# Kernel tuning notes

Hardware: AMD Instinct MI355X
Metric: run time of the kernel (lower is better)

## Reference

```python
import math
import jax, jax.numpy as jnp
import numpy as np

# --- dimensions ---
B = 32          # crystals
N_PER = 96      # building blocks per crystal
M = B * N_PER   # total nodes = 3072
H = 8           # no_heads
CH = 16         # c_hidden
PQK = 8         # no_qk_points
PV = 12         # no_v_points
CS = 256        # c_s
CZ = 128        # c_z
E = B * N_PER * N_PER  # dense intra-crystal edges = 294912
INV_SOFTPLUS_1 = 0.541324854612918


def _quat_to_rot(q):
    """Unit quaternion [M,4] -> rotation matrices [M,3,3]."""
    w, x, y, z = q[:, 0], q[:, 1], q[:, 2], q[:, 3]
    R = jnp.stack([
        1 - 2 * (y * y + z * z), 2 * (x * y - w * z), 2 * (x * z + w * y),
        2 * (x * y + w * z), 1 - 2 * (x * x + z * z), 2 * (y * z - w * x),
        2 * (x * z - w * y), 2 * (y * z + w * x), 1 - 2 * (x * x + y * y)],
        axis=-1)
    return R.reshape(-1, 3, 3)


def _lin_params(k, din, dout):
    kw, kb = jax.random.split(k)
    W = jax.random.normal(kw, (din, dout), jnp.float32) / np.sqrt(din).astype(np.float32)
    b = jax.random.normal(kb, (dout,), jnp.float32) * 0.01
    return W, b


def setup_inputs() -> dict:
    key = jax.random.key(0)
    ks = jax.random.split(key, 16)
    s = jax.random.normal(ks[0], (M, CS), jnp.float32)
    z = jax.random.normal(ks[1], (E, CZ), jnp.float32)
    quat = jax.random.normal(ks[2], (M, 4), jnp.float32)
    rot = _quat_to_rot(quat / jnp.linalg.norm(quat, axis=-1, keepdims=True))
    trans = jax.random.normal(ks[3], (M, 3), jnp.float32)
    L = jax.random.normal(ks[4], (B, 6), jnp.float32)
    # block-diagonal fully-connected intra-crystal edges
    i = np.repeat(np.arange(N_PER), N_PER)
    j = np.tile(np.arange(N_PER), N_PER)
    off = (np.arange(B) * N_PER)[:, None]
    src = (off + i[None, :]).reshape(-1)
    tgt = (off + j[None, :]).reshape(-1)
    edge_index = jnp.asarray(np.stack([src, tgt]), jnp.int32)
    num_bbs = jnp.full((B,), N_PER, jnp.int32)
    Wq, bq = _lin_params(ks[5], CS, H * CH)
    Wkv, bkv = _lin_params(ks[6], CS, 2 * H * CH)
    Wqp, bqp = _lin_params(ks[7], CS, H * PQK * 3)
    Wkvp, bkvp = _lin_params(ks[8], CS, H * (PQK + PV) * 3)
    Wb, bb = _lin_params(ks[9], CZ, H)
    Wl, bl = _lin_params(ks[10], 6, H)
    head_weights = INV_SOFTPLUS_1 + 0.1 * jax.random.normal(ks[11], (H,), jnp.float32)
    Wout, bout = _lin_params(ks[12], H * (CH + 3 * PV) + 6, CS)
    return dict(s=s, z=z, rot=rot, trans=trans, L=L,
                Wq=Wq, bq=bq, Wkv=Wkv, bkv=bkv, Wqp=Wqp, bqp=bqp,
                Wkvp=Wkvp, bkvp=bkvp, Wb=Wb, bb=bb, Wl=Wl, bl=bl,
                head_weights=head_weights, Wout=Wout, bout=bout,
                edge_index=edge_index, num_bbs=num_bbs)


def reference(s, z, rot, trans, L, Wq, bq, Wkv, bkv, Wqp, bqp, Wkvp, bkvp,
              Wb, bb, Wl, bl, head_weights, Wout, bout, edge_index, num_bbs):
    src, tgt = edge_index[0], edge_index[1]
    # scalar q/k/v
    q = (s @ Wq + bq).reshape(M, H, CH)
    kv = (s @ Wkv + bkv).reshape(M, H, 2 * CH)
    k, v = kv[..., :CH], kv[..., CH:]

    # point q/k/v: torch splits last dim into 3 coord chunks then stacks -> reshape (M,3,H,P)
    def points(W, bias, P):
        p = (s @ W + bias).reshape(M, 3, H, P).transpose(0, 2, 3, 1)  # [M,H,P,3]
        return jnp.einsum('mij,mhpj->mhpi', rot, p) + trans[:, None, None, :]

    q_pts = points(Wqp, bqp, PQK)                 # [M,H,PQK,3] in global frame
    kv_pts = points(Wkvp, bkvp, PQK + PV)         # [M,H,PQK+PV,3]
    k_pts, v_pts = kv_pts[:, :, :PQK], kv_pts[:, :, PQK:]

    b_pair = z @ Wb + bb                          # [E,H]
    batch_idx = jnp.repeat(jnp.arange(B), num_bbs, total_repeat_length=M)  # node -> crystal
    l_nodes = (L @ Wl + bl)[batch_idx]            # [M,H]

    # fused multi-term attention logits
    a = jnp.einsum('ehc,ehc->eh', q[tgt], k[src]) * math.sqrt(1.0 / (4 * CH))
    a = a + 0.5 * b_pair + 0.5 * l_nodes[src]
    disp = q_pts[tgt] - k_pts[src]                # [E,H,PQK,3]
    pt_att = jnp.sum(disp * disp, axis=-1)        # [E,H,PQK]
    hw = jax.nn.softplus(head_weights) * math.sqrt(1.0 / (4 * (PQK * 9.0 / 2)))
    a = a - 0.5 * jnp.sum(pt_att * hw[None, :, None], axis=-1)

    # segment softmax over incoming edges of each target node
    amax = jax.ops.segment_max(a, tgt, num_segments=M)
    ex = jnp.exp(a - amax[tgt])
    denom = jax.ops.segment_sum(ex, tgt, num_segments=M)
    attn = ex / denom[tgt]                        # [E,H]

    o = jax.ops.segment_sum(attn[..., None] * v[src], tgt, num_segments=M)
    o = o.reshape(M, H * CH)
    o_pt = jax.ops.segment_sum(attn[..., None, None] * v_pts[src], tgt, num_segments=M)
    o_pt = o_pt.reshape(M, H * PV, 3)
    o_l = L[batch_idx]                            # [M,6]
    o_feats = jnp.concatenate([o, o_pt[..., 0], o_pt[..., 1], o_pt[..., 2], o_l], axis=-1)
    return o_feats @ Wout + bout                  # [M,CS]
```

## Files before the change

### kernel.cpp

```cpp
#include <hip/hip_runtime.h>
#include <math.h>

#define B_    32
#define NPER_ 96
#define M_    3072
#define H_    8
#define CH_   16
#define PQK_  8
#define PV_   12
#define CS_   256
#define CZ_   128
#define E_    294912
#define NCAT_ 1056

template <bool ALIGN_A>
__global__ __launch_bounds__(256) void gemm64(const float* __restrict__ A,
                                              const float* __restrict__ W,
                                              const float* __restrict__ bias,
                                              float* __restrict__ C,
                                              int N, int K) {
  __shared__ float As[16][68];
  __shared__ float Bs[16][64];
  const int tid = threadIdx.x;
  const int tx = tid & 15, ty = tid >> 4;
  const int row0 = blockIdx.y * 64, col0 = blockIdx.x * 64;
  float acc[4][4] = {};

  for (int k0 = 0; k0 < K; k0 += 16) {
    {
      const int m = tid >> 2, k4 = (tid & 3) * 4;
      const int gk = k0 + k4;
      float a0 = 0.f, a1 = 0.f, a2 = 0.f, a3 = 0.f;
      if (ALIGN_A) {
        const float4 av = *reinterpret_cast<const float4*>(A + (size_t)(row0 + m) * K + gk);
        a0 = av.x; a1 = av.y; a2 = av.z; a3 = av.w;
      } else {
        const float* ap = A + (size_t)(row0 + m) * K;
        if (gk + 0 < K) a0 = ap[gk + 0];
        if (gk + 1 < K) a1 = ap[gk + 1];
        if (gk + 2 < K) a2 = ap[gk + 2];
        if (gk + 3 < K) a3 = ap[gk + 3];
      }
      As[k4 + 0][m] = a0; As[k4 + 1][m] = a1; As[k4 + 2][m] = a2; As[k4 + 3][m] = a3;
    }
    {
      const int kk = tid >> 4, n4 = (tid & 15) * 4;
      const int gk = k0 + kk, gn = col0 + n4;
      float4 bv; bv.x = 0.f; bv.y = 0.f; bv.z = 0.f; bv.w = 0.f;
      if (gk < K) {
        if (gn + 3 < N) {
          bv = *reinterpret_cast<const float4*>(W + (size_t)gk * N + gn);
        } else {
          const float* wp = W + (size_t)gk * N;
          if (gn + 0 < N) bv.x = wp[gn + 0];
          if (gn + 1 < N) bv.y = wp[gn + 1];
          if (gn + 2 < N) bv.z = wp[gn + 2];
          if (gn + 3 < N) bv.w = wp[gn + 3];
        }
      }
      *reinterpret_cast<float4*>(&Bs[kk][n4]) = bv;
    }
    __syncthreads();
#pragma unroll
    for (int kk = 0; kk < 16; ++kk) {
      const float4 a_ = *reinterpret_cast<const float4*>(&As[kk][ty * 4]);
      const float4 b_ = *reinterpret_cast<const float4*>(&Bs[kk][tx * 4]);
      acc[0][0] += a_.x * b_.x; acc[0][1] += a_.x * b_.y; acc[0][2] += a_.x * b_.z; acc[0][3] += a_.x * b_.w;
      acc[1][0] += a_.y * b_.x; acc[1][1] += a_.y * b_.y; acc[1][2] += a_.y * b_.z; acc[1][3] += a_.y * b_.w;
      acc[2][0] += a_.z * b_.x; acc[2][1] += a_.z * b_.y; acc[2][2] += a_.z * b_.z; acc[2][3] += a_.z * b_.w;
      acc[3][0] += a_.w * b_.x; acc[3][1] += a_.w * b_.y; acc[3][2] += a_.w * b_.z; acc[3][3] += a_.w * b_.w;
    }
    __syncthreads();
  }
#pragma unroll
  for (int i2 = 0; i2 < 4; ++i2) {
    const int gr = row0 + ty * 4 + i2;
#pragma unroll
    for (int j2 = 0; j2 < 4; ++j2) {
      const int gn = col0 + tx * 4 + j2;
      if (gn < N) C[(size_t)gr * N + gn] = acc[i2][j2] + bias[gn];
    }
  }
}

__global__ __launch_bounds__(256) void pack_w(const float* __restrict__ Wq,
                                              const float* __restrict__ Wkv,
                                              const float* __restrict__ Wqp,
                                              const float* __restrict__ Wkvp,
                                              const float* __restrict__ bq,
                                              const float* __restrict__ bkv,
                                              const float* __restrict__ bqp,
                                              const float* __restrict__ bkvp,
                                              float* __restrict__ Wcat,
                                              float* __restrict__ bcat) {
  const int t = blockIdx.x * 256 + threadIdx.x;
  if (t < 256 * NCAT_) {
    const int k = t / NCAT_, n = t - k * NCAT_;
    float v;
    if (n < 128)      v = Wq [k * 128 + n];
    else if (n < 384) v = Wkv[k * 256 + n - 128];
    else if (n < 576) v = Wqp[k * 192 + n - 384];
    else              v = Wkvp[k * 480 + n - 576];
    Wcat[t] = v;
  }
  if (t < NCAT_) {
    float v;
    if (t < 128)      v = bq[t];
    else if (t < 384) v = bkv[t - 128];
    else if (t < 576) v = bqp[t - 384];
    else              v = bkvp[t - 576];
    bcat[t] = v;
  }
}

__global__ __launch_bounds__(256) void rotate_pts(const float* __restrict__ praw,
                                                  const float* __restrict__ rot,
                                                  const float* __restrict__ trans,
                                                  const float* __restrict__ L,
                                                  float* __restrict__ qpts,
                                                  float* __restrict__ kpts,
                                                  float* __restrict__ vpts,
                                                  float* __restrict__ ofeat) {
  const int m = blockIdx.x;
  const int t = threadIdx.x;
  float R[9], T[3];
#pragma unroll
  for (int a = 0; a < 9; ++a) R[a] = rot[m * 9 + a];
#pragma unroll
  for (int a = 0; a < 3; ++a) T[a] = trans[m * 3 + a];
  const float* prow = praw + (size_t)m * NCAT_;

  if (t < 64) {
    const float x = prow[384 + t];
    const float y = prow[384 + 64 + t];
    const float z = prow[384 + 128 + t];
    const int h = t >> 3, p = t & 7;
    float* dst = qpts + ((size_t)(m * 8 + h) * 8 + p) * 3;
    dst[0] = R[0] * x + R[1] * y + R[2] * z + T[0];
    dst[1] = R[3] * x + R[4] * y + R[5] * z + T[1];
    dst[2] = R[6] * x + R[7] * y + R[8] * z + T[2];
  } else if (t < 224) {
    const int idx = t - 64;
    const float x = prow[576 + idx];
    const float y = prow[576 + 160 + idx];
    const float z = prow[576 + 320 + idx];
    const int h = idx / 20, p = idx % 20;
    const float o0 = R[0] * x + R[1] * y + R[2] * z + T[0];
    const float o1 = R[3] * x + R[4] * y + R[5] * z + T[1];
    const float o2 = R[6] * x + R[7] * y + R[8] * z + T[2];
    float* dst = (p < 8) ? (kpts + ((size_t)(m * 8 + h) * 8 + p) * 3)
                         : (vpts + ((size_t)(m * 8 + h) * 12 + (p - 8)) * 3);
    dst[0] = o0; dst[1] = o1; dst[2] = o2;
  } else if (t < 230) {
    ofeat[(size_t)m * 422 + 416 + (t - 224)] = L[(m / NPER_) * 6 + (t - 224)];
  }
}

__global__ __launch_bounds__(256) void bpair_kernel(const float* __restrict__ z,
                                                    const float* __restrict__ Wb,
                                                    const float* __restrict__ bb,
                                                    float* __restrict__ bT2) {
  const int l = threadIdx.x & 63;
  const int wave = blockIdx.x * 4 + (threadIdx.x >> 6);
  const int nw = gridDim.x * 4;
  const float4* W4 = reinterpret_cast<const float4*>(Wb);
  const float4 w0 = W4[l * 4 + 0];
  const float4 w1 = W4[l * 4 + 1];
  const float4 w2 = W4[l * 4 + 2];
  const float4 w3 = W4[l * 4 + 3];
  const int b0 = l & 1, b1 = (l >> 1) & 1, b2 = (l >> 2) & 1;
  const int myh = (b0 << 2) | (b1 << 1) | b2;
  const float mybb = bb[myh];
  const float2* z2 = reinterpret_cast<const float2*>(z);

  for (int row = wave; row < E_; row += nw) {
    const float2 zv = z2[(size_t)row * 64 + l];
    float a0 = zv.x * w0.x + zv.y * w2.x;
    float a1 = zv.x * w0.y + zv.y * w2.y;
    float a2 = zv.x * w0.z + zv.y * w2.z;
    float a3 = zv.x * w0.w + zv.y * w2.w;
    float a4 = zv.x * w1.x + zv.y * w3.x;
    float a5 = zv.x * w1.y + zv.y * w3.y;
    float a6 = zv.x * w1.z + zv.y * w3.z;
    float a7 = zv.x * w1.w + zv.y * w3.w;
    float s40 = (b0 ? a4 : a0) + __shfl_xor(b0 ? a0 : a4, 1);
    float s41 = (b0 ? a5 : a1) + __shfl_xor(b0 ? a1 : a5, 1);
    float s42 = (b0 ? a6 : a2) + __shfl_xor(b0 ? a2 : a6, 1);
    float s43 = (b0 ? a7 : a3) + __shfl_xor(b0 ? a3 : a7, 1);
    float s20 = (b1 ? s42 : s40) + __shfl_xor(b1 ? s40 : s42, 2);
    float s21 = (b1 ? s43 : s41) + __shfl_xor(b1 ? s41 : s43, 2);
    float s1 = (b2 ? s21 : s20) + __shfl_xor(b2 ? s20 : s21, 4);
    s1 += __shfl_xor(s1, 8);
    s1 += __shfl_xor(s1, 16);
    s1 += __shfl_xor(s1, 32);
    if (l < 8) {
      const int bb_ = row / 9216;
      const int el = row - bb_ * 9216;
      const int i = el / 96;
      const int jj = el - i * 96;
      bT2[(size_t)myh * E_ + (size_t)bb_ * 9216 + jj * 96 + i] = s1 + mybb;
    }
  }
}

__global__ __launch_bounds__(768, 3) void attn_kernel(const float* __restrict__ praw,
                                                      const float* __restrict__ qpts,
                                                      const float* __restrict__ kpts,
                                                      const float* __restrict__ vpts,
                                                      const float* __restrict__ bT2,
                                                      const float* __restrict__ L,
                                                      const float* __restrict__ Wl,
                                                      const float* __restrict__ bl,
                                                      const float* __restrict__ hwts,
                                                      float* __restrict__ ofeat) {
  const int b = blockIdx.x >> 3, h = blockIdx.x & 7;
  __shared__ float4 k4[96 * 5];
  __shared__ float4 v4[96 * 5];
  __shared__ float4 kp4[96 * 6];
  __shared__ float4 vp4[96 * 9];
  __shared__ float lds_b[96 * 100];
  const int tid = threadIdx.x;

  {
    const int i = tid >> 3, c = tid & 7;
    const float4* src = reinterpret_cast<const float4*>(praw + (size_t)(b * 96 + i) * NCAT_ + 128 + h * 32);
    if (c < 4) k4[i * 5 + c] = src[c];
    else       v4[i * 5 + (c - 4)] = src[c];
  }
  for (int t = tid; t < 96 * 6; t += 768) {
    const int i = t / 6, c = t - i * 6;
    kp4[t] = reinterpret_cast<const float4*>(kpts + ((size_t)(b * 96 + i) * 8 + h) * 24)[c];
  }
  for (int t = tid; t < 96 * 9; t += 768) {
    const int i = t / 9, c = t - i * 9;
    vp4[t] = reinterpret_cast<const float4*>(vpts + ((size_t)(b * 96 + i) * 8 + h) * 36)[c];
  }
  {
    const float4* g4 = reinterpret_cast<const float4*>(bT2 + (size_t)h * E_ + (size_t)b * 9216);
    for (int t = tid; t < 2304; t += 768) {
      const int jj = t / 24, c = t - jj * 24;
      reinterpret_cast<float4*>(lds_b + jj * 100)[c] = g4[t];
    }
  }
  __syncthreads();

  const int j = tid >> 3, qq = tid & 7;
  const int mj = b * 96 + j;

  float lb = bl[h];
#pragma unroll
  for (int d = 0; d < 6; ++d) lb += L[b * 6 + d] * Wl[d * 8 + h];
  const float c_l = 0.5f * lb;
  const float sp = logf(1.0f + __expf(hwts[h]));
  const float c_pt = 0.5f * sp * (1.0f / 12.0f);

  const float4* q4 = reinterpret_cast<const float4*>(praw + (size_t)mj * NCAT_ + h * 16);
  const float4 qa = q4[0], qb = q4[1], qc = q4[2], qd = q4[3];
  float qp[24];
  {
    const float4* qp4 = reinterpret_cast<const float4*>(qpts + ((size_t)mj * 8 + h) * 24);
#pragma unroll
    for (int c4 = 0; c4 < 6; ++c4) {
      const float4 v_ = qp4[c4];
      qp[c4 * 4 + 0] = v_.x; qp[c4 * 4 + 1] = v_.y; qp[c4 * 4 + 2] = v_.z; qp[c4 * 4 + 3] = v_.w;
    }
  }

  float lg[12];
  float mx = -3.0e38f;
#pragma unroll
  for (int s = 0; s < 12; ++s) {
    const int i = s * 8 + qq;
    const float4 ka = k4[i * 5 + 0], kb = k4[i * 5 + 1], kc = k4[i * 5 + 2], kd = k4[i * 5 + 3];
    float dot = qa.x * ka.x + qa.y * ka.y + qa.z * ka.z + qa.w * ka.w
              + qb.x * kb.x + qb.y * kb.y + qb.z * kb.z + qb.w * kb.w
              + qc.x * kc.x + qc.y * kc.y + qc.z * kc.z + qc.w * kc.w
              + qd.x * kd.x + qd.y * kd.y + qd.z * kd.z + qd.w * kd.w;
    float pd = 0.f;
#pragma unroll
    for (int c4 = 0; c4 < 6; ++c4) {
      const float4 kp = kp4[i * 6 + c4];
      const float d0 = qp[c4 * 4 + 0] - kp.x;
      const float d1 = qp[c4 * 4 + 1] - kp.y;
      const float d2 = qp[c4 * 4 + 2] - kp.z;
      const float d3 = qp[c4 * 4 + 3] - kp.w;
      pd += d0 * d0 + d1 * d1 + d2 * d2 + d3 * d3;
    }
    const float lv = dot * 0.125f + 0.5f * lds_b[j * 100 + i] + c_l - c_pt * pd;
    lg[s] = lv;
    mx = fmaxf(mx, lv);
  }
  mx = fmaxf(mx, __shfl_xor(mx, 1));
  mx = fmaxf(mx, __shfl_xor(mx, 2));
  mx = fmaxf(mx, __shfl_xor(mx, 4));
  float sum = 0.f;
#pragma unroll
  for (int s = 0; s < 12; ++s) { lg[s] = __expf(lg[s] - mx); sum += lg[s]; }
  sum += __shfl_xor(sum, 1);
  sum += __shfl_xor(sum, 2);
  sum += __shfl_xor(sum, 4);
  const float inv = 1.0f / sum;

  float acco[16] = {};
  float accp[36] = {};
#pragma unroll
  for (int s = 0; s < 12; ++s) {
    const int i = s * 8 + qq;
    const float w = lg[s];
#pragma unroll
    for (int c4 = 0; c4 < 4; ++c4) {
      const float4 vv = v4[i * 5 + c4];
      acco[c4 * 4 + 0] += w * vv.x; acco[c4 * 4 + 1] += w * vv.y;
      acco[c4 * 4 + 2] += w * vv.z; acco[c4 * 4 + 3] += w * vv.w;
    }
#pragma unroll
    for (int c4 = 0; c4 < 9; ++c4) {
      const float4 pv = vp4[i * 9 + c4];
      accp[c4 * 4 + 0] += w * pv.x; accp[c4 * 4 + 1] += w * pv.y;
      accp[c4 * 4 + 2] += w * pv.z; accp[c4 * 4 + 3] += w * pv.w;
    }
  }
#pragma unroll
  for (int u = 0; u < 16; ++u) {
    acco[u] += __shfl_xor(acco[u], 1); acco[u] += __shfl_xor(acco[u], 2); acco[u] += __shfl_xor(acco[u], 4);
  }
#pragma unroll
  for (int u = 0; u < 36; ++u) {
    accp[u] += __shfl_xor(accp[u], 1); accp[u] += __shfl_xor(accp[u], 2); accp[u] += __shfl_xor(accp[u], 4);
  }

  if (qq == 0) {
    float* orow = ofeat + (size_t)mj * 422;
#pragma unroll
    for (int c = 0; c < 16; ++c) orow[h * 16 + c] = acco[c] * inv;
#pragma unroll
    for (int d = 0; d < 3; ++d)
#pragma unroll
      for (int p = 0; p < 12; ++p)
        orow[128 + d * 96 + h * 12 + p] = accp[p * 3 + d] * inv;
  }
}

extern "C" void kernel_launch(void* const* d_in, const int* in_sizes, int n_in,
                              void* d_out, int out_size, void* d_ws, size_t ws_size,
                              hipStream_t stream) {
  const float* s     = (const float*)d_in[0];
  const float* z     = (const float*)d_in[1];
  const float* rot   = (const float*)d_in[2];
  const float* trans = (const float*)d_in[3];
  const float* L     = (const float*)d_in[4];
  const float* Wq    = (const float*)d_in[5];
  const float* bq    = (const float*)d_in[6];
  const float* Wkv   = (const float*)d_in[7];
  const float* bkv   = (const float*)d_in[8];
  const float* Wqp   = (const float*)d_in[9];
  const float* bqp   = (const float*)d_in[10];
  const float* Wkvp  = (const float*)d_in[11];
  const float* bkvp  = (const float*)d_in[12];
  const float* Wb    = (const float*)d_in[13];
  const float* bb    = (const float*)d_in[14];
  const float* Wl    = (const float*)d_in[15];
  const float* bl    = (const float*)d_in[16];
  const float* hwts  = (const float*)d_in[17];
  const float* Wout  = (const float*)d_in[18];
  const float* bout  = (const float*)d_in[19];
  float* out = (float*)d_out;
  float* ws  = (float*)d_ws;

  float* praw  = ws;
  float* qpts  = praw  + 3244032;
  float* kpts  = qpts  + 589824;
  float* vpts  = kpts  + 589824;
  float* ofeat = vpts  + 884736;
  float* bT2   = ofeat + 1296384;
  float* Wcat  = bT2   + 2359296;
  float* bcat  = Wcat  + 270336;

  pack_w<<<(256 * NCAT_ + 255) / 256, 256, 0, stream>>>(Wq, Wkv, Wqp, Wkvp, bq, bkv, bqp, bkvp, Wcat, bcat);
  gemm64<true ><<<dim3(17, 48), 256, 0, stream>>>(s, Wcat, bcat, praw, NCAT_, 256);
  rotate_pts<<<M_, 256, 0, stream>>>(praw, rot, trans, L, qpts, kpts, vpts, ofeat);
  bpair_kernel<<<2048, 256, 0, stream>>>(z, Wb, bb, bT2);
  attn_kernel<<<256, 768, 0, stream>>>(praw, qpts, kpts, vpts, bT2, L, Wl, bl, hwts, ofeat);
  gemm64<false><<<dim3(4, 48), 256, 0, stream>>>(ofeat, Wout, bout, out, 256, 422);
}
```

Measured before the change: 370.0 us.

## Coalesce bias-pair transpose via LDS, split attention blocks, pad output features

The pair-bias kernel now gives each block one (crystal, target) column and stages the per-head results in shared memory, so global writes of the transposed bias are coalesced instead of scattered. The attention kernel is split into two half-blocks per (crystal, head), which doubles the grid and halves the bias staging in shared memory. The concatenated feature buffer is padded to a stride of 432 so the output GEMM can take the aligned float4 load path, with a separate K bound for the weights so the padded columns contribute nothing. The GEMM epilogue also writes float4 vectors. The split means the K/V tiles are loaded twice, and the bias kernel now launches many small blocks.

Result: slower. 379.8 us (+2.6%).

```diff
diff --git a/kernel.cpp b/kernel.cpp
--- a/kernel.cpp
+++ b/kernel.cpp
@@ -12,13 +12,14 @@
 #define CZ_   128
 #define E_    294912
 #define NCAT_ 1056
+#define OF_   432
 
 template <bool ALIGN_A>
 __global__ __launch_bounds__(256) void gemm64(const float* __restrict__ A,
                                               const float* __restrict__ W,
                                               const float* __restrict__ bias,
                                               float* __restrict__ C,
-                                              int N, int K) {
+                                              int N, int K, int KW) {
   __shared__ float As[16][68];
   __shared__ float Bs[16][64];
   const int tid = threadIdx.x;
@@ -47,7 +48,7 @@
       const int kk = tid >> 4, n4 = (tid & 15) * 4;
       const int gk = k0 + kk, gn = col0 + n4;
       float4 bv; bv.x = 0.f; bv.y = 0.f; bv.z = 0.f; bv.w = 0.f;
-      if (gk < K) {
+      if (gk < KW) {
         if (gn + 3 < N) {
           bv = *reinterpret_cast<const float4*>(W + (size_t)gk * N + gn);
         } else {
@@ -72,13 +73,22 @@
     }
     __syncthreads();
   }
+  const int gn0 = col0 + tx * 4;
 #pragma unroll
   for (int i2 = 0; i2 < 4; ++i2) {
     const int gr = row0 + ty * 4 + i2;
-#pragma unroll
-    for (int j2 = 0; j2 < 4; ++j2) {
-      const int gn = col0 + tx * 4 + j2;
-      if (gn < N) C[(size_t)gr * N + gn] = acc[i2][j2] + bias[gn];
+    if (gn0 + 3 < N) {
+      const float4 bsv = *reinterpret_cast<const float4*>(bias + gn0);
+      float4 cv;
+      cv.x = acc[i2][0] + bsv.x; cv.y = acc[i2][1] + bsv.y;
+      cv.z = acc[i2][2] + bsv.z; cv.w = acc[i2][3] + bsv.w;
+      *reinterpret_cast<float4*>(C + (size_t)gr * N + gn0) = cv;
+    } else {
+#pragma unroll
+      for (int j2 = 0; j2 < 4; ++j2) {
+        const int gn = gn0 + j2;
+        if (gn < N) C[(size_t)gr * N + gn] = acc[i2][j2] + bias[gn];
+      }
     }
   }
 }
@@ -152,7 +162,7 @@
                          : (vpts + ((size_t)(m * 8 + h) * 12 + (p - 8)) * 3);
     dst[0] = o0; dst[1] = o1; dst[2] = o2;
   } else if (t < 230) {
-    ofeat[(size_t)m * 422 + 416 + (t - 224)] = L[(m / NPER_) * 6 + (t - 224)];
+    ofeat[(size_t)m * OF_ + 416 + (t - 224)] = L[(m / NPER_) * 6 + (t - 224)];
   }
 }
 
@@ -160,9 +170,11 @@
                                                     const float* __restrict__ Wb,
                                                     const float* __restrict__ bb,
                                                     float* __restrict__ bT2) {
+  __shared__ float lds_out[96 * 9];
+  const int bid = blockIdx.x;
+  const int b = bid / 96, j = bid - b * 96;
   const int l = threadIdx.x & 63;
-  const int wave = blockIdx.x * 4 + (threadIdx.x >> 6);
-  const int nw = gridDim.x * 4;
+  const int w = threadIdx.x >> 6;
   const float4* W4 = reinterpret_cast<const float4*>(Wb);
   const float4 w0 = W4[l * 4 + 0];
   const float4 w1 = W4[l * 4 + 1];
@@ -173,8 +185,10 @@
   const float mybb = bb[myh];
   const float2* z2 = reinterpret_cast<const float2*>(z);
 
-  for (int row = wave; row < E_; row += nw) {
-    const float2 zv = z2[(size_t)row * 64 + l];
+#pragma unroll 1
+  for (int i = w; i < 96; i += 4) {
+    const size_t e = (size_t)b * 9216 + (size_t)i * 96 + j;
+    const float2 zv = z2[e * 64 + l];
     float a0 = zv.x * w0.x + zv.y * w2.x;
     float a1 = zv.x * w0.y + zv.y * w2.y;
     float a2 = zv.x * w0.z + zv.y * w2.z;
@@ -193,17 +207,16 @@
     s1 += __shfl_xor(s1, 8);
     s1 += __shfl_xor(s1, 16);
     s1 += __shfl_xor(s1, 32);
-    if (l < 8) {
-      const int bb_ = row / 9216;
-      const int el = row - bb_ * 9216;
-      const int i = el / 96;
-      const int jj = el - i * 96;
-      bT2[(size_t)myh * E_ + (size_t)bb_ * 9216 + jj * 96 + i] = s1 + mybb;
-    }
-  }
-}
-
-__global__ __launch_bounds__(768, 3) void attn_kernel(const float* __restrict__ praw,
+    if (l < 8) lds_out[i * 9 + myh] = s1 + mybb;
+  }
+  __syncthreads();
+  for (int idx = threadIdx.x; idx < 768; idx += 256) {
+    const int h = idx / 96, i = idx - h * 96;
+    bT2[(size_t)h * E_ + (size_t)b * 9216 + j * 96 + i] = lds_out[i * 9 + h];
+  }
+}
+
+__global__ __launch_bounds__(384, 3) void attn_kernel(const float* __restrict__ praw,
                                                       const float* __restrict__ qpts,
                                                       const float* __restrict__ kpts,
                                                       const float* __restrict__ vpts,
@@ -213,38 +226,41 @@
                                                       const float* __restrict__ bl,
                                                       const float* __restrict__ hwts,
                                                       float* __restrict__ ofeat) {
-  const int b = blockIdx.x >> 3, h = blockIdx.x & 7;
+  const int bid = blockIdx.x;
+  const int b = bid >> 4, h = (bid >> 1) & 7, half = bid & 1;
+  const int j0 = half * 48;
   __shared__ float4 k4[96 * 5];
   __shared__ float4 v4[96 * 5];
   __shared__ float4 kp4[96 * 6];
   __shared__ float4 vp4[96 * 9];
-  __shared__ float lds_b[96 * 100];
+  __shared__ float lds_b[48 * 100];
   const int tid = threadIdx.x;
 
-  {
-    const int i = tid >> 3, c = tid & 7;
+  for (int t = tid; t < 96 * 8; t += 384) {
+    const int i = t >> 3, c = t & 7;
     const float4* src = reinterpret_cast<const float4*>(praw + (size_t)(b * 96 + i) * NCAT_ + 128 + h * 32);
     if (c < 4) k4[i * 5 + c] = src[c];
     else       v4[i * 5 + (c - 4)] = src[c];
   }
-  for (int t = tid; t < 96 * 6; t += 768) {
+  for (int t = tid; t < 96 * 6; t += 384) {
     const int i = t / 6, c = t - i * 6;
     kp4[t] = reinterpret_cast<const float4*>(kpts + ((size_t)(b * 96 + i) * 8 + h) * 24)[c];
   }
-  for (int t = tid; t < 96 * 9; t += 768) {
+  for (int t = tid; t < 96 * 9; t += 384) {
     const int i = t / 9, c = t - i * 9;
     vp4[t] = reinterpret_cast<const float4*>(vpts + ((size_t)(b * 96 + i) * 8 + h) * 36)[c];
   }
   {
-    const float4* g4 = reinterpret_cast<const float4*>(bT2 + (size_t)h * E_ + (size_t)b * 9216);
-    for (int t = tid; t < 2304; t += 768) {
+    const float4* g4 = reinterpret_cast<const float4*>(bT2 + (size_t)h * E_ + (size_t)b * 9216 + (size_t)j0 * 96);
+    for (int t = tid; t < 48 * 24; t += 384) {
       const int jj = t / 24, c = t - jj * 24;
       reinterpret_cast<float4*>(lds_b + jj * 100)[c] = g4[t];
     }
   }
   __syncthreads();
 
-  const int j = tid >> 3, qq = tid & 7;
+  const int jl = tid >> 3, qq = tid & 7;
+  const int j = j0 + jl;
   const int mj = b * 96 + j;
 
   float lb = bl[h];
@@ -286,7 +302,7 @@
       const float d3 = qp[c4 * 4 + 3] - kp.w;
       pd += d0 * d0 + d1 * d1 + d2 * d2 + d3 * d3;
     }
-    const float lv = dot * 0.125f + 0.5f * lds_b[j * 100 + i] + c_l - c_pt * pd;
+    const float lv = dot * 0.125f + 0.5f * lds_b[jl * 100 + i] + c_l - c_pt * pd;
     lg[s] = lv;
     mx = fmaxf(mx, lv);
   }
@@ -330,7 +346,7 @@
   }
 
   if (qq == 0) {
-    float* orow = ofeat + (size_t)mj * 422;
+    float* orow = ofeat + (size_t)mj * OF_;
 #pragma unroll
     for (int c = 0; c < 16; ++c) orow[h * 16 + c] = acco[c] * inv;
 #pragma unroll
@@ -372,14 +388,14 @@
   float* kpts  = qpts  + 589824;
   float* vpts  = kpts  + 589824;
   float* ofeat = vpts  + 884736;
-  float* bT2   = ofeat + 1296384;
+  float* bT2   = ofeat + 1327104;
   float* Wcat  = bT2   + 2359296;
   float* bcat  = Wcat  + 270336;
 
   pack_w<<<(256 * NCAT_ + 255) / 256, 256, 0, stream>>>(Wq, Wkv, Wqp, Wkvp, bq, bkv, bqp, bkvp, Wcat, bcat);
-  gemm64<true ><<<dim3(17, 48), 256, 0, stream>>>(s, Wcat, bcat, praw, NCAT_, 256);
+  gemm64<true ><<<dim3(17, 48), 256, 0, stream>>>(s, Wcat, bcat, praw, NCAT_, 256, 256);
   rotate_pts<<<M_, 256, 0, stream>>>(praw, rot, trans, L, qpts, kpts, vpts, ofeat);
-  bpair_kernel<<<2048, 256, 0, stream>>>(z, Wb, bb, bT2);
-  attn_kernel<<<256, 768, 0, stream>>>(praw, qpts, kpts, vpts, bT2, L, Wl, bl, hwts, ofeat);
-  gemm64<false><<<dim3(4, 48), 256, 0, stream>>>(ofeat, Wout, bout, out, 256, 422);
-}
+  bpair_kernel<<<B_ * NPER_, 256, 0, stream>>>(z, Wb, bb, bT2);
+  attn_kernel<<<512, 384, 0, stream>>>(praw, qpts, kpts, vpts, bT2, L, Wl, bl, hwts, ofeat);
+  gemm64<true ><<<dim3(4, 48), 256, 0, stream>>>(ofeat, Wout, bout, out, 256, OF_, 422);
+}
```
